# Kernel tuning notes

Measured on AMD Instinct MI355X. Metric: run time of the kernel, lower is better.

Reference implementation:

```python
import jax, jax.numpy as jnp
import numpy as np
import math

B, S, HID = 16, 512, 768
NUM_LABELS = 9
NUM_HEADS = 4
HEAD_DIM = HID // NUM_HEADS
MAX_REL = 5
B_PERSON = 1
I_PERSON = 2
LN_EPS = 1e-5


def setup_inputs() -> dict:
    key = jax.random.key(0)
    ks = jax.random.split(key, 16)
    w = lambda k, shp: jax.random.normal(k, shp, dtype=jnp.float32) * 0.02
    return {
        "sequence_output": jax.random.normal(ks[0], (B, S, HID), dtype=jnp.float32),
        "Wq": w(ks[1], (HID, HID)), "bq": jnp.zeros((HID,), jnp.float32),
        "Wk": w(ks[2], (HID, HID)), "bk": jnp.zeros((HID,), jnp.float32),
        "Wv": w(ks[3], (HID, HID)), "bv": jnp.zeros((HID,), jnp.float32),
        "Wo": w(ks[4], (HID, HID)), "bo": jnp.zeros((HID,), jnp.float32),
        "ln_g": jnp.ones((HID,), jnp.float32), "ln_b": jnp.zeros((HID,), jnp.float32),
        "Ws": w(ks[5], (HID, NUM_LABELS)), "bs": jnp.zeros((NUM_LABELS,), jnp.float32),
        "entity_bias": w(ks[6], (NUM_LABELS,)),
    }


def _heads(x):
    # [B,S,HID] -> [B,H,S,D]
    return x.reshape(B, S, NUM_HEADS, HEAD_DIM).transpose(0, 2, 1, 3)


def reference(sequence_output, Wq, bq, Wk, bk, Wv, bv, Wo, bo, ln_g, ln_b, Ws, bs, entity_bias):
    x = sequence_output
    q = _heads(x @ Wq + bq)
    k = _heads(x @ Wk + bk)
    v = _heads(x @ Wv + bv)

    scores = jnp.einsum("bhqd,bhkd->bhqk", q, k)
    # relative position bias: exp(-0.1 * clamp(|i-j|, 0, MAX_REL)), broadcast over b,h
    idx = jnp.arange(S, dtype=jnp.float32)
    dist = jnp.abs(idx[None, :] - idx[:, None])  # [S,S]
    rel_bias = jnp.exp(-0.1 * jnp.clip(dist, 0.0, float(MAX_REL)))
    dist_mask = -0.1 * dist
    scores = (scores + rel_bias) / math.sqrt(HEAD_DIM) + dist_mask
    probs = jax.nn.softmax(scores, axis=-1)  # dropout is identity in eval

    ctx = jnp.einsum("bhqk,bhkd->bhqd", probs, v)
    ctx = ctx.transpose(0, 2, 1, 3).reshape(B, S, HID)
    out = ctx @ Wo + bo

    h = x + out
    mu = jnp.mean(h, axis=-1, keepdims=True)
    var = jnp.mean(jnp.square(h - mu), axis=-1, keepdims=True)
    h = (h - mu) * jax.lax.rsqrt(var + LN_EPS) * ln_g + ln_b

    span_logits = h @ Ws + bs  # [B,S,L]
    # vectorized entity-bias post-process: the torch loop adds entity_bias[I_PERSON]
    # TWICE to final_logits[:, j, I_PERSON] whenever argmax(span_logits[:, j-1]) == B_PERSON
    prev_is_b = jnp.argmax(span_logits[:, :-1], axis=-1) == B_PERSON  # [B,S-1]
    bump = jnp.where(prev_is_b, 2.0 * entity_bias[I_PERSON], 0.0)
    final_logits = span_logits.at[:, 1:, I_PERSON].add(bump)
    return final_logits
```

## Files before the change

kernel.cpp:

```cpp
#include <hip/hip_runtime.h>
#include <math.h>

#define SEQ 512
#define HID 768
#define NBATCH 16
#define ROWS 8192
#define INV_SQRT_D 0.07216878364870323f

typedef short s8v __attribute__((ext_vector_type(8)));
typedef _Float16 h8v __attribute__((ext_vector_type(8)));
typedef float f4v __attribute__((ext_vector_type(4)));
typedef unsigned short u16;

__device__ __forceinline__ u16 f2h(float f) {
  _Float16 h = (_Float16)f;
  return __builtin_bit_cast(u16, h);
}

__device__ __forceinline__ void llds16(const u16* g, u16* l) {
  __builtin_amdgcn_global_load_lds(
      (const __attribute__((address_space(1))) void*)g,
      (__attribute__((address_space(3))) void*)l, 16, 0, 0);
}

template <int KSTEPS>
__device__ __forceinline__ void mm_core128(
    const u16* __restrict__ A, const int lda,
    const u16* __restrict__ B, const int ldb,
    u16* lds, f4v (&acc)[4][4])
{
  const int tid = threadIdx.x;
  const int w = tid >> 6, ln = tid & 63;
  const u16* src = (w >> 1) ? B : A;
  const int ld = (w >> 1) ? ldb : lda;
  const int half = w & 1;
  const int srow = ln >> 2;
  const int csw  = ((ln & 3) - (ln >> 3)) & 3;
  const int ml = ln & 15;
  const int fo2 = (((ln >> 4) + ((ln >> 1) & 3)) & 3) * 8;
  const int wr = (w >> 1) * 64, wc = (w & 1) * 64;

  const u16* gp[4];
  u16* lp[4];
#pragma unroll
  for (int t = 0; t < 4; ++t) {
    const int row = half * 64 + t * 16 + srow;
    gp[t] = src + (size_t)row * ld + csw * 8;
    lp[t] = lds + (w >> 1) * 4096 + half * 2048 + t * 512;
  }

  for (int kp = 0; kp < KSTEPS / 2; ++kp) {
    const int k0 = kp * 64;
    __syncthreads();
#pragma unroll
    for (int t = 0; t < 4; ++t) {
      llds16(gp[t] + k0,      lp[t]);
      llds16(gp[t] + k0 + 32, lp[t] + 8192);
    }
    __syncthreads();
#pragma unroll
    for (int sub = 0; sub < 2; ++sub) {
      const int so = sub * 8192;
      h8v a[4], b[4];
#pragma unroll
      for (int i = 0; i < 4; ++i)
        a[i] = *(const h8v*)&lds[so + (wr + i * 16 + ml) * 32 + fo2];
#pragma unroll
      for (int j = 0; j < 4; ++j)
        b[j] = *(const h8v*)&lds[so + 4096 + (wc + j * 16 + ml) * 32 + fo2];
#pragma unroll
      for (int i = 0; i < 4; ++i)
#pragma unroll
        for (int j = 0; j < 4; ++j)
          acc[i][j] = __builtin_amdgcn_mfma_f32_16x16x32_f16(a[i], b[j], acc[i][j], 0, 0, 0);
    }
  }
}

__global__ __launch_bounds__(256) void splitx(const float* __restrict__ x,
                                              u16* __restrict__ xh)
{
  const int i = blockIdx.x * 256 + threadIdx.x;
  const float4 v = ((const float4*)x)[i];
  ((ushort4*)xh)[i] = make_ushort4(f2h(v.x), f2h(v.y), f2h(v.z), f2h(v.w));
}

__global__ __launch_bounds__(256) void wsplit(
    const float* __restrict__ Wq, const float* __restrict__ Wk,
    const float* __restrict__ Wv, const float* __restrict__ Wo,
    u16* __restrict__ WTh)
{
  __shared__ float t[32][33];
  const int z = blockIdx.z;
  const float* W = (z == 0) ? Wq : (z == 1) ? Wk : (z == 2) ? Wv : Wo;
  const int n0 = blockIdx.x * 32, k0 = blockIdx.y * 32;
  const int tx = threadIdx.x & 31, ty = threadIdx.x >> 5;
#pragma unroll
  for (int i = 0; i < 4; ++i)
    t[ty + 8 * i][tx] = W[(size_t)(k0 + ty + 8 * i) * HID + n0 + tx];
  __syncthreads();
#pragma unroll
  for (int i = 0; i < 4; ++i) {
    const float v = t[tx][ty + 8 * i];
    const size_t idx = (size_t)z * HID * HID + (size_t)(n0 + ty + 8 * i) * HID + k0 + tx;
    WTh[idx] = f2h(v);
  }
}

__global__ __launch_bounds__(256, 3) void qkv_mm(
    const u16* __restrict__ xh, const u16* __restrict__ WTh,
    const float* __restrict__ bq, const float* __restrict__ bk, const float* __restrict__ bv,
    u16* __restrict__ qh, u16* __restrict__ kh, u16* __restrict__ vTh)
{
  __shared__ u16 lds[17408];
  const int id = blockIdx.x;
  const int xcd = id & 7;
  const int s = id >> 3;
  const int bx = s % 6;
  const int yl = (s / 6) & 7;
  const int z  = s / 48;
  const int bm = (yl * 8 + xcd) * 128;
  const int bn = bx * 128;
  const size_t wtoff = (size_t)z * HID * HID + (size_t)bn * HID;
  f4v acc[4][4];
#pragma unroll
  for (int i = 0; i < 4; ++i)
#pragma unroll
    for (int j = 0; j < 4; ++j) acc[i][j] = (f4v)0.f;
  mm_core128<24>(xh + (size_t)bm * HID, HID, WTh + wtoff, HID, lds, acc);
  const int tid = threadIdx.x, w = tid >> 6, ln = tid & 63;
  const int ml = ln & 15, quad = ln >> 4;
  const int wr = (w >> 1) * 64, wc = (w & 1) * 64;
  if (z == 2) {
    __syncthreads();
#pragma unroll
    for (int i = 0; i < 4; ++i)
#pragma unroll
      for (int j = 0; j < 4; ++j) {
        const int ncol = wc + j * 16 + ml;
        const float bv_ = bv[bn + ncol];
#pragma unroll
        for (int r = 0; r < 4; ++r) {
          const int srow = wr + i * 16 + quad * 4 + r;
          lds[ncol * 136 + srow] = f2h(acc[i][j][r] + bv_);
        }
      }
    __syncthreads();
    u16* vb = vTh + (size_t)(bm >> 9) * HID * SEQ;
    const int sq0 = bm & 511;
    const int c8 = (tid & 15) * 8;
#pragma unroll
    for (int p = 0; p < 8; ++p) {
      const int nl = p * 16 + (tid >> 4);
      const s8v val = *(const s8v*)&lds[nl * 136 + c8];
      *(s8v*)&vb[(size_t)(bn + nl) * SEQ + sq0 + c8] = val;
    }
  } else {
    const float* bias = (z == 0) ? bq : bk;
    u16* dst = (z == 0) ? qh : kh;
#pragma unroll
    for (int i = 0; i < 4; ++i)
#pragma unroll
      for (int j = 0; j < 4; ++j) {
        const int gcol = bn + wc + j * 16 + ml;
        const float bv_ = bias[gcol];
#pragma unroll
        for (int r = 0; r < 4; ++r) {
          const int grow = bm + wr + i * 16 + quad * 4 + r;
          dst[(size_t)grow * HID + gcol] = f2h(acc[i][j][r] + bv_);
        }
      }
  }
}

__global__ __launch_bounds__(256, 2) void attn_fused(
    const u16* __restrict__ qh, const u16* __restrict__ kh,
    const u16* __restrict__ vTh, u16* __restrict__ ch)
{
  __shared__ u16 lds[31232];
  __shared__ float gtab[1024];
  __shared__ float red[4][32];
  const int f = blockIdx.x;
  const int xcd = f & 7, s = f >> 3;
  const int z = xcd * 8 + (s >> 3);
  const int bm = (s & 7) * 64;
  const int b = z >> 2, hh = z & 3;
  const int tid = threadIdx.x, w = tid >> 6, ln = tid & 63;
  const int ml = ln & 15, quad = ln >> 4;
  const int rh = w >> 1, ch2 = w & 1;

  for (int t = tid; t < 1023; t += 256) {
    const float fd = fabsf((float)(t - 511));
    gtab[t] = INV_SQRT_D * __expf(-0.1f * fminf(fd, 5.0f)) - 0.1f * fd;
  }

  const u16* qbase = qh + (size_t)(b * SEQ + bm + rh * 32) * HID + hh * 192;
  const u16* kbase = kh + (size_t)b * SEQ * HID + hh * 192;
  const u16* vbase = vTh + (size_t)b * HID * SEQ + (size_t)(hh * 192) * SEQ;

  h8v qf[2][6];
#pragma unroll
  for (int i = 0; i < 2; ++i)
#pragma unroll
    for (int ks = 0; ks < 6; ++ks)
      qf[i][ks] = *(const h8v*)(qbase + (size_t)(i * 16 + ml) * HID + ks * 32 + quad * 8);

  int koff[6], kldso[6], voff[6], vldso[6];
#pragma unroll
  for (int c = 0; c < 6; ++c) {
    const int cc = c * 256 + tid;
    const int krow = cc / 24, kcol = cc % 24;
    koff[c]  = krow * HID + kcol * 8;
    kldso[c] = krow * 200 + kcol * 8;
    const int vrow = cc >> 3, vcol = cc & 7;
    voff[c]  = vrow * SEQ + vcol * 8;
    vldso[c] = 12800 + vrow * 72 + vcol * 8;
  }
  s8v kc[6], vc[6];
#pragma unroll
  for (int c = 0; c < 6; ++c) {
    kc[c] = *(const s8v*)(kbase + koff[c]);
    vc[c] = *(const s8v*)(vbase + voff[c]);
  }

  f4v acc2[2][6];
#pragma unroll
  for (int i = 0; i < 2; ++i)
#pragma unroll
    for (int jj = 0; jj < 6; ++jj) acc2[i][jj] = (f4v)0.f;
  float rsum[2][4];
#pragma unroll
  for (int i = 0; i < 2; ++i)
#pragma unroll
    for (int r = 0; r < 4; ++r) rsum[i][r] = 0.f;

  for (int j = 0; j < 8; ++j) {
    __syncthreads();
#pragma unroll
    for (int c = 0; c < 6; ++c) {
      *(s8v*)&lds[kldso[c]] = kc[c];
      *(s8v*)&lds[vldso[c]] = vc[c];
    }
    __syncthreads();
    if (j < 7) {
      const int ko = (j + 1) * 64;
#pragma unroll
      for (int c = 0; c < 6; ++c) {
        kc[c] = *(const s8v*)(kbase + (size_t)ko * HID + koff[c]);
        vc[c] = *(const s8v*)(vbase + ko + voff[c]);
      }
    }
    f4v sacc[2][2];
    sacc[0][0] = (f4v)0.f; sacc[0][1] = (f4v)0.f;
    sacc[1][0] = (f4v)0.f; sacc[1][1] = (f4v)0.f;
    __builtin_amdgcn_s_setprio(1);
#pragma unroll
    for (int ks = 0; ks < 6; ++ks) {
      h8v kf0 = *(const h8v*)&lds[(ch2 * 32 + ml) * 200 + ks * 32 + quad * 8];
      h8v kf1 = *(const h8v*)&lds[(ch2 * 32 + 16 + ml) * 200 + ks * 32 + quad * 8];
      sacc[0][0] = __builtin_amdgcn_mfma_f32_16x16x32_f16(qf[0][ks], kf0, sacc[0][0], 0, 0, 0);
      sacc[1][0] = __builtin_amdgcn_mfma_f32_16x16x32_f16(qf[1][ks], kf0, sacc[1][0], 0, 0, 0);
      sacc[0][1] = __builtin_amdgcn_mfma_f32_16x16x32_f16(qf[0][ks], kf1, sacc[0][1], 0, 0, 0);
      sacc[1][1] = __builtin_amdgcn_mfma_f32_16x16x32_f16(qf[1][ks], kf1, sacc[1][1], 0, 0, 0);
    }
    __builtin_amdgcn_s_setprio(0);
#pragma unroll
    for (int i = 0; i < 2; ++i)
#pragma unroll
      for (int j2 = 0; j2 < 2; ++j2) {
        const int lcol = ch2 * 32 + j2 * 16 + ml;
        const int scolg = j * 64 + lcol;
#pragma unroll
        for (int r = 0; r < 4; ++r) {
          const int lrow = rh * 32 + i * 16 + quad * 4 + r;
          const float g = gtab[bm + lrow - scolg + 511];
          const float p = __expf(fmaf(sacc[i][j2][r], INV_SQRT_D, g));
          rsum[i][r] += p;
          lds[26624 + lrow * 72 + lcol] = f2h(p);
        }
      }
    __syncthreads();
    __builtin_amdgcn_s_setprio(1);
#pragma unroll
    for (int ks = 0; ks < 2; ++ks) {
      h8v pf[2], vf[6];
#pragma unroll
      for (int i = 0; i < 2; ++i)
        pf[i] = *(const h8v*)&lds[26624 + (rh * 32 + i * 16 + ml) * 72 + ks * 32 + quad * 8];
#pragma unroll
      for (int jj = 0; jj < 6; ++jj)
        vf[jj] = *(const h8v*)&lds[12800 + (ch2 * 96 + jj * 16 + ml) * 72 + ks * 32 + quad * 8];
#pragma unroll
      for (int i = 0; i < 2; ++i)
#pragma unroll
        for (int jj = 0; jj < 6; ++jj)
          acc2[i][jj] = __builtin_amdgcn_mfma_f32_16x16x32_f16(pf[i], vf[jj], acc2[i][jj], 0, 0, 0);
    }
    __builtin_amdgcn_s_setprio(0);
  }

#pragma unroll
  for (int i = 0; i < 2; ++i)
#pragma unroll
    for (int r = 0; r < 4; ++r) {
      float t = rsum[i][r];
#pragma unroll
      for (int o = 1; o < 16; o <<= 1) t += __shfl_xor(t, o, 64);
      rsum[i][r] = t;
    }
  if (ml == 0) {
#pragma unroll
    for (int i = 0; i < 2; ++i)
#pragma unroll
      for (int r = 0; r < 4; ++r) red[w][i * 16 + quad * 4 + r] = rsum[i][r];
  }
  __syncthreads();

#pragma unroll
  for (int i = 0; i < 2; ++i)
#pragma unroll
    for (int r = 0; r < 4; ++r) {
      const int lr = i * 16 + quad * 4 + r;
      const float is = 1.0f / (red[rh * 2][lr] + red[rh * 2 + 1][lr]);
      const int m = bm + rh * 32 + lr;
#pragma unroll
      for (int jj = 0; jj < 6; ++jj) {
        const int gcol = hh * 192 + ch2 * 96 + jj * 16 + ml;
        ch[(size_t)(b * SEQ + m) * HID + gcol] = f2h(acc2[i][jj][r] * is);
      }
    }
}

__global__ __launch_bounds__(256, 3) void proj_mm(
    const u16* __restrict__ ch, const u16* __restrict__ WTh,
    const float* __restrict__ bo, const float* __restrict__ x, float* __restrict__ h)
{
  __shared__ u16 lds[16384];
  const int id = blockIdx.x;
  const int xcd = id & 7;
  const int s = id >> 3;
  const int bx = s % 6;
  const int yl = s / 6;
  const int bm = (yl * 8 + xcd) * 128;
  const int bn = bx * 128;
  const size_t wtoff = (size_t)3 * HID * HID + (size_t)bn * HID;
  f4v acc[4][4];
#pragma unroll
  for (int i = 0; i < 4; ++i)
#pragma unroll
    for (int j = 0; j < 4; ++j) acc[i][j] = (f4v)0.f;
  mm_core128<24>(ch + (size_t)bm * HID, HID, WTh + wtoff, HID, lds, acc);
  const int tid = threadIdx.x, w = tid >> 6, ln = tid & 63;
  const int ml = ln & 15, quad = ln >> 4;
  const int wr = (w >> 1) * 64, wc = (w & 1) * 64;
#pragma unroll
  for (int i = 0; i < 4; ++i)
#pragma unroll
    for (int j = 0; j < 4; ++j) {
      const int gcol = bn + wc + j * 16 + ml;
      const float bv_ = bo[gcol];
#pragma unroll
      for (int r = 0; r < 4; ++r) {
        const int grow = bm + wr + i * 16 + quad * 4 + r;
        const size_t idx = (size_t)grow * HID + gcol;
        h[idx] = acc[i][j][r] + bv_ + x[idx];
      }
    }
}

__global__ __launch_bounds__(256) void ln_logits_kernel(
    const float* __restrict__ h, const float* __restrict__ g,
    const float* __restrict__ bta, const float* __restrict__ Ws,
    const float* __restrict__ bsv, float* __restrict__ span)
{
  const int row = blockIdx.x;
  const int tid = threadIdx.x;
  const float* hr = h + (size_t)row * HID;
  const float x0 = hr[tid], x1 = hr[tid + 256], x2 = hr[tid + 512];
  float s = x0 + x1 + x2;
  float sq = x0 * x0 + x1 * x1 + x2 * x2;
#pragma unroll
  for (int o = 32; o > 0; o >>= 1) { s += __shfl_down(s, o, 64); sq += __shfl_down(sq, o, 64); }
  __shared__ float red[8];
  __shared__ float smu, srs;
  const int wid = tid >> 6, lid = tid & 63;
  if (lid == 0) { red[wid] = s; red[4 + wid] = sq; }
  __syncthreads();
  if (tid == 0) {
    const float ts = red[0] + red[1] + red[2] + red[3];
    const float tq = red[4] + red[5] + red[6] + red[7];
    const float mu = ts / 768.0f;
    const float var = tq / 768.0f - mu * mu;
    smu = mu; srs = rsqrtf(var + 1e-5f);
  }
  __syncthreads();
  const float mu = smu, rs = srs;
  const float n0 = (x0 - mu) * rs * g[tid] + bta[tid];
  const float n1 = (x1 - mu) * rs * g[tid + 256] + bta[tid + 256];
  const float n2 = (x2 - mu) * rs * g[tid + 512] + bta[tid + 512];
  float pl[9];
#pragma unroll
  for (int l = 0; l < 9; ++l)
    pl[l] = n0 * Ws[(size_t)tid * 9 + l]
          + n1 * Ws[(size_t)(tid + 256) * 9 + l]
          + n2 * Ws[(size_t)(tid + 512) * 9 + l];
#pragma unroll
  for (int l = 0; l < 9; ++l)
#pragma unroll
    for (int o = 32; o > 0; o >>= 1) pl[l] += __shfl_down(pl[l], o, 64);
  __shared__ float lred[4][9];
  if (lid == 0) {
#pragma unroll
    for (int l = 0; l < 9; ++l) lred[wid][l] = pl[l];
  }
  __syncthreads();
  if (tid < 9) {
    span[(size_t)row * 9 + tid] =
        lred[0][tid] + lred[1][tid] + lred[2][tid] + lred[3][tid] + bsv[tid];
  }
}

__global__ __launch_bounds__(256) void bump_kernel(
    const float* __restrict__ span, const float* __restrict__ eb, float* __restrict__ out)
{
  const int idx = blockIdx.x * 256 + threadIdx.x;
  if (idx >= ROWS) return;
  const int j = idx & (SEQ - 1);
  const float* sl = span + (size_t)idx * 9;
  float v[9];
#pragma unroll
  for (int l = 0; l < 9; ++l) v[l] = sl[l];
  if (j >= 1) {
    const float* sp = sl - 9;
    float m = sp[0]; int am = 0;
#pragma unroll
    for (int l = 1; l < 9; ++l) { const float t = sp[l]; if (t > m) { m = t; am = l; } }
    if (am == 1) v[2] += 2.0f * eb[2];
  }
#pragma unroll
  for (int l = 0; l < 9; ++l) out[(size_t)idx * 9 + l] = v[l];
}

extern "C" void kernel_launch(void* const* d_in, const int* in_sizes, int n_in,
                              void* d_out, int out_size, void* d_ws, size_t ws_size,
                              hipStream_t stream)
{
  (void)in_sizes; (void)n_in; (void)out_size; (void)ws_size;
  const float* x   = (const float*)d_in[0];
  const float* Wq  = (const float*)d_in[1];
  const float* bq  = (const float*)d_in[2];
  const float* Wk  = (const float*)d_in[3];
  const float* bk  = (const float*)d_in[4];
  const float* Wv  = (const float*)d_in[5];
  const float* bv  = (const float*)d_in[6];
  const float* Wo  = (const float*)d_in[7];
  const float* bo  = (const float*)d_in[8];
  const float* lng = (const float*)d_in[9];
  const float* lnb = (const float*)d_in[10];
  const float* Ws  = (const float*)d_in[11];
  const float* bs  = (const float*)d_in[12];
  const float* eb  = (const float*)d_in[13];
  float* out = (float*)d_out;

  char* ws = (char*)d_ws;
  u16* xh  = (u16*)(ws + 0);
  u16* WTh = (u16*)(ws + 25165824);
  u16* qh  = (u16*)(ws + 34603008);
  u16* kh  = (u16*)(ws + 59768832);
  u16* vTh = (u16*)(ws + 84934656);
  float* hb = (float*)(ws + 84934656);
  float* spanb = (float*)(ws + 152043520);
  u16* ctxh = qh;

  splitx<<<dim3(1572864 / 256), 256, 0, stream>>>(x, xh);
  wsplit<<<dim3(24, 24, 4), 256, 0, stream>>>(Wq, Wk, Wv, Wo, WTh);
  qkv_mm<<<dim3(1152), 256, 0, stream>>>(xh, WTh, bq, bk, bv, qh, kh, vTh);
  attn_fused<<<dim3(512), 256, 0, stream>>>(qh, kh, vTh, ctxh);
  proj_mm<<<dim3(384), 256, 0, stream>>>(ctxh, WTh, bo, x, hb);
  ln_logits_kernel<<<dim3(ROWS), 256, 0, stream>>>(hb, lng, lnb, Ws, bs, spanb);
  bump_kernel<<<dim3(ROWS / 256), 256, 0, stream>>>(spanb, eb, out);
}
```

Measured before the change: 219.1 us.

## Stage Q/K epilogue through LDS, raise occupancy, wave-per-row LayerNorm

The Q/K epilogue of qkv_mm now writes results into LDS and then emits coalesced 16-byte row stores instead of scattered 2-byte global stores. The LDS buffer grows slightly to fit the staged tile. Launch bounds for qkv_mm and proj_mm go from 3 to 4 blocks per CU, which may limit registers and cause spills. The LN+logits kernel now handles one row per wave with float4 loads and xor-shuffle reductions, dropping its block-level syncs and shared-memory reductions.

```diff
diff --git a/kernel.cpp b/kernel.cpp
--- a/kernel.cpp
+++ b/kernel.cpp
@@ -107,12 +107,12 @@
   }
 }
 
-__global__ __launch_bounds__(256, 3) void qkv_mm(
+__global__ __launch_bounds__(256, 4) void qkv_mm(
     const u16* __restrict__ xh, const u16* __restrict__ WTh,
     const float* __restrict__ bq, const float* __restrict__ bk, const float* __restrict__ bv,
     u16* __restrict__ qh, u16* __restrict__ kh, u16* __restrict__ vTh)
 {
-  __shared__ u16 lds[17408];
+  __shared__ u16 lds[18432];
   const int id = blockIdx.x;
   const int xcd = id & 7;
   const int s = id >> 3;
@@ -158,18 +158,27 @@
   } else {
     const float* bias = (z == 0) ? bq : bk;
     u16* dst = (z == 0) ? qh : kh;
+    __syncthreads();
 #pragma unroll
     for (int i = 0; i < 4; ++i)
 #pragma unroll
       for (int j = 0; j < 4; ++j) {
-        const int gcol = bn + wc + j * 16 + ml;
-        const float bv_ = bias[gcol];
+        const int col = wc + j * 16 + ml;
+        const float bv_ = bias[bn + col];
 #pragma unroll
         for (int r = 0; r < 4; ++r) {
-          const int grow = bm + wr + i * 16 + quad * 4 + r;
-          dst[(size_t)grow * HID + gcol] = f2h(acc[i][j][r] + bv_);
+          const int row = wr + i * 16 + quad * 4 + r;
+          lds[row * 132 + col] = f2h(acc[i][j][r] + bv_);
         }
       }
+    __syncthreads();
+    const int c8 = (tid & 15) * 8;
+#pragma unroll
+    for (int p = 0; p < 8; ++p) {
+      const int rl = p * 16 + (tid >> 4);
+      const s8v val = *(const s8v*)&lds[rl * 132 + c8];
+      *(s8v*)&dst[(size_t)(bm + rl) * HID + bn + c8] = val;
+    }
   }
 }
 
@@ -331,7 +340,7 @@
     }
 }
 
-__global__ __launch_bounds__(256, 3) void proj_mm(
+__global__ __launch_bounds__(256, 4) void proj_mm(
     const u16* __restrict__ ch, const u16* __restrict__ WTh,
     const float* __restrict__ bo, const float* __restrict__ x, float* __restrict__ h)
 {
@@ -373,50 +382,48 @@
     const float* __restrict__ bta, const float* __restrict__ Ws,
     const float* __restrict__ bsv, float* __restrict__ span)
 {
-  const int row = blockIdx.x;
-  const int tid = threadIdx.x;
+  const int row = blockIdx.x * 4 + (threadIdx.x >> 6);
+  const int lane = threadIdx.x & 63;
   const float* hr = h + (size_t)row * HID;
-  const float x0 = hr[tid], x1 = hr[tid + 256], x2 = hr[tid + 512];
-  float s = x0 + x1 + x2;
-  float sq = x0 * x0 + x1 * x1 + x2 * x2;
-#pragma unroll
-  for (int o = 32; o > 0; o >>= 1) { s += __shfl_down(s, o, 64); sq += __shfl_down(sq, o, 64); }
-  __shared__ float red[8];
-  __shared__ float smu, srs;
-  const int wid = tid >> 6, lid = tid & 63;
-  if (lid == 0) { red[wid] = s; red[4 + wid] = sq; }
-  __syncthreads();
-  if (tid == 0) {
-    const float ts = red[0] + red[1] + red[2] + red[3];
-    const float tq = red[4] + red[5] + red[6] + red[7];
-    const float mu = ts / 768.0f;
-    const float var = tq / 768.0f - mu * mu;
-    smu = mu; srs = rsqrtf(var + 1e-5f);
-  }
-  __syncthreads();
-  const float mu = smu, rs = srs;
-  const float n0 = (x0 - mu) * rs * g[tid] + bta[tid];
-  const float n1 = (x1 - mu) * rs * g[tid + 256] + bta[tid + 256];
-  const float n2 = (x2 - mu) * rs * g[tid + 512] + bta[tid + 512];
+  float4 v[3];
+#pragma unroll
+  for (int sgm = 0; sgm < 3; ++sgm) v[sgm] = ((const float4*)hr)[sgm * 64 + lane];
+  float s = 0.f, sq = 0.f;
+#pragma unroll
+  for (int sgm = 0; sgm < 3; ++sgm) {
+    s  += v[sgm].x + v[sgm].y + v[sgm].z + v[sgm].w;
+    sq += v[sgm].x * v[sgm].x + v[sgm].y * v[sgm].y
+        + v[sgm].z * v[sgm].z + v[sgm].w * v[sgm].w;
+  }
+#pragma unroll
+  for (int o = 1; o < 64; o <<= 1) { s += __shfl_xor(s, o, 64); sq += __shfl_xor(sq, o, 64); }
+  const float mu = s / 768.0f;
+  const float rs = rsqrtf(sq / 768.0f - mu * mu + 1e-5f);
   float pl[9];
 #pragma unroll
+  for (int l = 0; l < 9; ++l) pl[l] = 0.f;
+#pragma unroll
+  for (int sgm = 0; sgm < 3; ++sgm) {
+    const int c0 = sgm * 256 + lane * 4;
+    const float4 gg = ((const float4*)g)[sgm * 64 + lane];
+    const float4 bb = ((const float4*)bta)[sgm * 64 + lane];
+    const float n0 = (v[sgm].x - mu) * rs * gg.x + bb.x;
+    const float n1 = (v[sgm].y - mu) * rs * gg.y + bb.y;
+    const float n2 = (v[sgm].z - mu) * rs * gg.z + bb.z;
+    const float n3 = (v[sgm].w - mu) * rs * gg.w + bb.w;
+    const float* w0 = Ws + (size_t)c0 * 9;
+#pragma unroll
+    for (int l = 0; l < 9; ++l)
+      pl[l] += n0 * w0[l] + n1 * w0[9 + l] + n2 * w0[18 + l] + n3 * w0[27 + l];
+  }
+#pragma unroll
   for (int l = 0; l < 9; ++l)
-    pl[l] = n0 * Ws[(size_t)tid * 9 + l]
-          + n1 * Ws[(size_t)(tid + 256) * 9 + l]
-          + n2 * Ws[(size_t)(tid + 512) * 9 + l];
-#pragma unroll
-  for (int l = 0; l < 9; ++l)
-#pragma unroll
-    for (int o = 32; o > 0; o >>= 1) pl[l] += __shfl_down(pl[l], o, 64);
-  __shared__ float lred[4][9];
-  if (lid == 0) {
-#pragma unroll
-    for (int l = 0; l < 9; ++l) lred[wid][l] = pl[l];
-  }
-  __syncthreads();
-  if (tid < 9) {
-    span[(size_t)row * 9 + tid] =
-        lred[0][tid] + lred[1][tid] + lred[2][tid] + lred[3][tid] + bsv[tid];
+#pragma unroll
+    for (int o = 1; o < 64; o <<= 1) pl[l] += __shfl_xor(pl[l], o, 64);
+  if (lane == 0) {
+    float* sp = span + (size_t)row * 9;
+#pragma unroll
+    for (int l = 0; l < 9; ++l) sp[l] = pl[l] + bsv[l];
   }
 }
 
@@ -477,6 +484,6 @@
   qkv_mm<<<dim3(1152), 256, 0, stream>>>(xh, WTh, bq, bk, bv, qh, kh, vTh);
   attn_fused<<<dim3(512), 256, 0, stream>>>(qh, kh, vTh, ctxh);
   proj_mm<<<dim3(384), 256, 0, stream>>>(ctxh, WTh, bo, x, hb);
-  ln_logits_kernel<<<dim3(ROWS), 256, 0, stream>>>(hb, lng, lnb, Ws, bs, spanb);
+  ln_logits_kernel<<<dim3(ROWS / 4), 256, 0, stream>>>(hb, lng, lnb, Ws, bs, spanb);
   bump_kernel<<<dim3(ROWS / 256), 256, 0, stream>>>(spanb, eb, out);
 }
```

Measured after the change: 201.2 us. 1.09x faster.
